# Optimization experiments

Hardware: AMD Instinct MI355X
Metric: run time of the kernel (lower is better)

## Reference

```python
import jax, jax.numpy as jnp
import numpy as np

N, D, P, Q = 4096, 512, 8, 32
MARGIN = 1.0
L2_WEIGHT = 0.005
EPS = 1e-6  # torch.nn.PairwiseDistance default eps, added to the difference


def setup_inputs() -> dict:
    key = jax.random.key(0)
    k1, k2, k3 = jax.random.split(key, 3)
    batch = jax.random.normal(k1, (N, D), dtype=jnp.float32)
    anchors = jnp.arange(N, dtype=jnp.int64) if jax.config.jax_enable_x64 else jnp.arange(N, dtype=jnp.int32)
    pos_idx = jax.random.randint(k2, (N, P), 0, N)
    neg_idx = jax.random.randint(k3, (N, Q), 0, N)
    return {"batch": batch, "anchors": anchors, "pos_idx": pos_idx, "neg_idx": neg_idx}


def reference(batch, anchors, pos_idx, neg_idx):
    # batch: [N, D]; anchors: [N]; pos_idx: [N, P]; neg_idx: [N, Q]
    a = batch[anchors]                       # [N, D]
    # PairwiseDistance(p=2): (sum |x - y + eps|^2)^(1/2)
    d_pos = jnp.sqrt(jnp.sum((a[:, None, :] - batch[pos_idx] + EPS) ** 2, axis=-1))  # [N, P]
    d_neg = jnp.sqrt(jnp.sum((a[:, None, :] - batch[neg_idx] + EPS) ** 2, axis=-1))  # [N, Q]
    pos_term = jax.scipy.special.logsumexp(d_pos, axis=1)            # [N]
    neg_term = jax.scipy.special.logsumexp(MARGIN - d_neg, axis=1)   # [N]
    per_anchor = jax.nn.relu(pos_term + neg_term)                    # [N]
    l2_term = L2_WEIGHT * jnp.mean(jnp.sqrt(jnp.sum(batch ** 2, axis=1)))
    return jnp.mean(per_anchor) + l2_term
```

## Files before the change

kernel.cpp:

```cpp
#include <hip/hip_runtime.h>
#include <math.h>
#include <float.h>

#define NN 4096
#define DD 512
#define PP 8
#define QQ 32
#define NB_TOT 40
#define NPW 10
constexpr float MARGIN = 1.0f;
constexpr float L2W    = 0.005f;
constexpr float EPS    = 1e-6f;

typedef _Float16 half8 __attribute__((ext_vector_type(8)));

#define WS_NORM (NN * DD / 2)
#define WS_RES  (WS_NORM + NN)

__device__ inline float wave_reduce_sum(float v) {
    v += __shfl_xor(v, 32, 64);
    v += __shfl_xor(v, 16, 64);
    v += __shfl_xor(v,  8, 64);
    v += __shfl_xor(v,  4, 64);
    v += __shfl_xor(v,  2, 64);
    v += __shfl_xor(v,  1, 64);
    return v;
}

__device__ inline float wave_reduce_max(float v) {
    v = fmaxf(v, __shfl_xor(v, 32, 64));
    v = fmaxf(v, __shfl_xor(v, 16, 64));
    v = fmaxf(v, __shfl_xor(v,  8, 64));
    v = fmaxf(v, __shfl_xor(v,  4, 64));
    v = fmaxf(v, __shfl_xor(v,  2, 64));
    v = fmaxf(v, __shfl_xor(v,  1, 64));
    return v;
}

__global__ __launch_bounds__(256) void convert_kernel(
    const float4* __restrict__ batch4,
    half8*        __restrict__ hb,
    float*        __restrict__ norms)
{
    const int row  = blockIdx.x * 4 + (threadIdx.x >> 6);
    const int lane = threadIdx.x & 63;

    const float4 v0 = batch4[row * 128 + lane * 2];
    const float4 v1 = batch4[row * 128 + lane * 2 + 1];

    half8 h;
    h[0] = (_Float16)v0.x; h[1] = (_Float16)v0.y;
    h[2] = (_Float16)v0.z; h[3] = (_Float16)v0.w;
    h[4] = (_Float16)v1.x; h[5] = (_Float16)v1.y;
    h[6] = (_Float16)v1.z; h[7] = (_Float16)v1.w;
    hb[row * 64 + lane] = h;

    float s = v0.x*v0.x + v0.y*v0.y + v0.z*v0.z + v0.w*v0.w
            + v1.x*v1.x + v1.y*v1.y + v1.z*v1.z + v1.w*v1.w;
    s = wave_reduce_sum(s);
    if (lane == 0) norms[row] = sqrtf(s);
}

__global__ __launch_bounds__(256) void dist_kernel(
    const half8* __restrict__ hb,
    const int*   __restrict__ anchors,
    const int*   __restrict__ pos_idx,
    const int*   __restrict__ neg_idx,
    const float* __restrict__ norms,
    float*       __restrict__ res)
{
    const int i    = blockIdx.x;
    const int tid  = threadIdx.x;
    const int lane = tid & 63;
    const int wave = tid >> 6;
    const int jb   = wave * NPW;

    __shared__ float dist[NB_TOT];

    const int arow = anchors[i];
    const half8 ah = hb[(size_t)arow * 64 + lane];
    float a[8];
    #pragma unroll
    for (int k = 0; k < 8; ++k) a[k] = (float)ah[k] + EPS;

    int idxs[NPW];
    #pragma unroll
    for (int t = 0; t < NPW; ++t) {
        const int j = jb + t;
        idxs[t] = (j < PP) ? pos_idx[i * PP + j] : neg_idx[i * QQ + (j - PP)];
    }

    half8 bh[NPW];
    #pragma unroll
    for (int t = 0; t < NPW; ++t)
        bh[t] = hb[(size_t)idxs[t] * 64 + lane];

    float s[NPW];
    #pragma unroll
    for (int t = 0; t < NPW; ++t) {
        float acc = 0.0f;
        #pragma unroll
        for (int k = 0; k < 8; ++k) {
            const float d = a[k] - (float)bh[t][k];
            acc = fmaf(d, d, acc);
        }
        s[t] = acc;
    }

    #pragma unroll
    for (int t = 0; t < NPW; ++t) s[t] = wave_reduce_sum(s[t]);

    float v = s[0];
    #pragma unroll
    for (int t = 1; t < NPW; ++t) v = (lane == t) ? s[t] : v;
    if (lane < NPW) dist[jb + lane] = sqrtf(v);

    __syncthreads();

    if (wave == 0) {
        const float d = (lane < NB_TOT) ? dist[lane] : 0.0f;

        const bool pact = (lane < PP);
        const float pm = wave_reduce_max(pact ? d : -FLT_MAX);
        const float ps = wave_reduce_sum(pact ? expf(d - pm) : 0.0f);
        const float pos_term = pm + logf(ps);

        const bool nact = (lane >= PP) && (lane < NB_TOT);
        const float nv = MARGIN - d;
        const float nm = wave_reduce_max(nact ? nv : -FLT_MAX);
        const float ns = wave_reduce_sum(nact ? expf(nv - nm) : 0.0f);
        const float neg_term = nm + logf(ns);

        if (lane == 0)
            res[i] = fmaxf(0.0f, pos_term + neg_term) + L2W * norms[i];
    }
}

__global__ __launch_bounds__(256) void reduce_kernel(
    const float* __restrict__ res, float* __restrict__ out)
{
    const int tid  = threadIdx.x;
    const int lane = tid & 63;
    const int wave = tid >> 6;

    const float4* __restrict__ w4 = reinterpret_cast<const float4*>(res);
    float s = 0.0f;
    #pragma unroll
    for (int k = 0; k < 4; ++k) {
        const float4 v = w4[tid + 256 * k];
        s += v.x + v.y + v.z + v.w;
    }
    s = wave_reduce_sum(s);

    __shared__ float part[4];
    if (lane == 0) part[wave] = s;
    __syncthreads();
    if (tid == 0)
        out[0] = (part[0] + part[1] + part[2] + part[3]) * (1.0f / (float)NN);
}

extern "C" void kernel_launch(void* const* d_in, const int* in_sizes, int n_in,
                              void* d_out, int out_size, void* d_ws, size_t ws_size,
                              hipStream_t stream) {
    const float* batch   = (const float*)d_in[0];
    const int*   anchors = (const int*)d_in[1];
    const int*   pos_idx = (const int*)d_in[2];
    const int*   neg_idx = (const int*)d_in[3];
    float*       wsf     = (float*)d_ws;
    float*       out     = (float*)d_out;

    half8* hb    = (half8*)wsf;
    float* norms = wsf + WS_NORM;
    float* res   = wsf + WS_RES;

    convert_kernel<<<NN / 4, 256, 0, stream>>>((const float4*)batch, hb, norms);
    dist_kernel<<<NN, 256, 0, stream>>>(hb, anchors, pos_idx, neg_idx, norms, res);
    reduce_kernel<<<1, 256, 0, stream>>>(res, out);
}
```

Before: 85.11 us.

## Fuse final reduction via atomics, use transposed shuffle reduce with 5 waves

Removes the separate reduce kernel by having each dist block atomically add its scaled per-anchor loss into the output, which the convert kernel zeroes first. The dist kernel now runs 320 threads (5 waves of 8 neighbours each) and reduces the 8 partial sums with a butterfly/transpose shuffle pattern, using fewer shuffles than 8 independent full wave reductions. This saves one launch and some shuffle work, at the cost of 4096 contended atomics on one address and a nondeterministic summation order.

```diff
diff --git a/kernel.cpp b/kernel.cpp
--- a/kernel.cpp
+++ b/kernel.cpp
@@ -7,7 +7,7 @@
 #define PP 8
 #define QQ 32
 #define NB_TOT 40
-#define NPW 10
+#define NPW 8
 constexpr float MARGIN = 1.0f;
 constexpr float L2W    = 0.005f;
 constexpr float EPS    = 1e-6f;
@@ -15,7 +15,6 @@
 typedef _Float16 half8 __attribute__((ext_vector_type(8)));
 
 #define WS_NORM (NN * DD / 2)
-#define WS_RES  (WS_NORM + NN)
 
 __device__ inline float wave_reduce_sum(float v) {
     v += __shfl_xor(v, 32, 64);
@@ -40,7 +39,8 @@
 __global__ __launch_bounds__(256) void convert_kernel(
     const float4* __restrict__ batch4,
     half8*        __restrict__ hb,
-    float*        __restrict__ norms)
+    float*        __restrict__ norms,
+    float*        __restrict__ out)
 {
     const int row  = blockIdx.x * 4 + (threadIdx.x >> 6);
     const int lane = threadIdx.x & 63;
@@ -59,15 +59,16 @@
             + v1.x*v1.x + v1.y*v1.y + v1.z*v1.z + v1.w*v1.w;
     s = wave_reduce_sum(s);
     if (lane == 0) norms[row] = sqrtf(s);
+    if (blockIdx.x == 0 && threadIdx.x == 0) out[0] = 0.0f;
 }
 
-__global__ __launch_bounds__(256) void dist_kernel(
+__global__ __launch_bounds__(320) void dist_kernel(
     const half8* __restrict__ hb,
     const int*   __restrict__ anchors,
     const int*   __restrict__ pos_idx,
     const int*   __restrict__ neg_idx,
     const float* __restrict__ norms,
-    float*       __restrict__ res)
+    float*       __restrict__ out)
 {
     const int i    = blockIdx.x;
     const int tid  = threadIdx.x;
@@ -107,13 +108,34 @@
         s[t] = acc;
     }
 
+    float h4[4];
     #pragma unroll
-    for (int t = 0; t < NPW; ++t) s[t] = wave_reduce_sum(s[t]);
+    for (int t = 0; t < 4; ++t) {
+        const bool hi = (lane & 32) != 0;
+        const float send = hi ? s[t] : s[t + 4];
+        const float recv = __shfl_xor(send, 32, 64);
+        h4[t] = (hi ? s[t + 4] : s[t]) + recv;
+    }
+    float h2[2];
+    #pragma unroll
+    for (int t = 0; t < 2; ++t) {
+        const bool hi = (lane & 16) != 0;
+        const float send = hi ? h4[t] : h4[t + 2];
+        const float recv = __shfl_xor(send, 16, 64);
+        h2[t] = (hi ? h4[t + 2] : h4[t]) + recv;
+    }
+    float h1;
+    {
+        const bool hi = (lane & 8) != 0;
+        const float send = hi ? h2[0] : h2[1];
+        const float recv = __shfl_xor(send, 8, 64);
+        h1 = (hi ? h2[1] : h2[0]) + recv;
+    }
+    h1 += __shfl_xor(h1, 4, 64);
+    h1 += __shfl_xor(h1, 2, 64);
+    h1 += __shfl_xor(h1, 1, 64);
 
-    float v = s[0];
-    #pragma unroll
-    for (int t = 1; t < NPW; ++t) v = (lane == t) ? s[t] : v;
-    if (lane < NPW) dist[jb + lane] = sqrtf(v);
+    if ((lane & 7) == 0) dist[jb + (lane >> 3)] = sqrtf(h1);
 
     __syncthreads();
 
@@ -131,32 +153,11 @@
         const float ns = wave_reduce_sum(nact ? expf(nv - nm) : 0.0f);
         const float neg_term = nm + logf(ns);
 
-        if (lane == 0)
-            res[i] = fmaxf(0.0f, pos_term + neg_term) + L2W * norms[i];
+        if (lane == 0) {
+            const float val = fmaxf(0.0f, pos_term + neg_term) + L2W * norms[i];
+            atomicAdd(out, val * (1.0f / (float)NN));
+        }
     }
-}
-
-__global__ __launch_bounds__(256) void reduce_kernel(
-    const float* __restrict__ res, float* __restrict__ out)
-{
-    const int tid  = threadIdx.x;
-    const int lane = tid & 63;
-    const int wave = tid >> 6;
-
-    const float4* __restrict__ w4 = reinterpret_cast<const float4*>(res);
-    float s = 0.0f;
-    #pragma unroll
-    for (int k = 0; k < 4; ++k) {
-        const float4 v = w4[tid + 256 * k];
-        s += v.x + v.y + v.z + v.w;
-    }
-    s = wave_reduce_sum(s);
-
-    __shared__ float part[4];
-    if (lane == 0) part[wave] = s;
-    __syncthreads();
-    if (tid == 0)
-        out[0] = (part[0] + part[1] + part[2] + part[3]) * (1.0f / (float)NN);
 }
 
 extern "C" void kernel_launch(void* const* d_in, const int* in_sizes, int n_in,
@@ -171,9 +172,7 @@
 
     half8* hb    = (half8*)wsf;
     float* norms = wsf + WS_NORM;
-    float* res   = wsf + WS_RES;
 
-    convert_kernel<<<NN / 4, 256, 0, stream>>>((const float4*)batch, hb, norms);
-    dist_kernel<<<NN, 256, 0, stream>>>(hb, anchors, pos_idx, neg_idx, norms, res);
-    reduce_kernel<<<1, 256, 0, stream>>>(res, out);
+    convert_kernel<<<NN / 4, 256, 0, stream>>>((const float4*)batch, hb, norms, out);
+    dist_kernel<<<NN, 320, 0, stream>>>(hb, anchors, pos_idx, neg_idx, norms, out);
 }
```

Result: slower. 122.8 us (+44.2%).
